# Kernel tuning notes

Measured on AMD Instinct MI355X. Metric: run time of the kernel, lower is better.

## Reference

```python
import jax, jax.numpy as jnp
import numpy as np

B, C, NS, NT = 8, 256, 16384, 2048
KQ = 64            # self-attention key/query dim
D = 64             # cond_conv_feat_dim
W0, W1, W2 = D * D, D * D, D * 1   # dynamic weight sizes (predict_mask=True)
B0, B1, B2 = D, D, 1
CTRL = W0 + W1 + W2 + B0 + B1 + B2  # 8385


def setup_inputs() -> dict:
    key = jax.random.key(0)
    ks = jax.random.split(key, 9)
    return {
        "scene_feat": jax.random.normal(ks[0], (B, C, NS), jnp.float32),
        "template_feat": jax.random.normal(ks[1], (B, C, NT), jnp.float32),
        # SelfAttention 1x1-conv (= linear over channels) weights
        "q_w": jax.random.normal(ks[2], (KQ, C), jnp.float32) * 0.02,
        "k_w": jax.random.normal(ks[3], (KQ, C), jnp.float32) * 0.02,
        "v_w": jax.random.normal(ks[4], (C, C), jnp.float32) * 0.02,
        # projection head of SimpleAggregator: Conv1d(3*C -> D, k=1) + ReLU
        "proj_w": jax.random.normal(ks[5], (D, 3 * C), jnp.float32) * 0.02,
        "proj_b": jnp.zeros((D,), jnp.float32),
        # controller head: Linear(C -> CTRL), init normal(std=0.01), bias 0
        "ctrl_w": jax.random.normal(ks[6], (CTRL, C), jnp.float32) * 0.01,
        "ctrl_b": jnp.zeros((CTRL,), jnp.float32),
    }


def _self_attention(x, q_w, k_w, v_w):
    # x: [B, C, N] -> [B, C_out, N]
    q = jnp.einsum("kc,bcn->bnk", q_w, x)          # [B, N, KQ]
    k = jnp.einsum("kc,bcn->bkn", k_w, x)          # [B, KQ, N]
    v = jnp.einsum("oc,bcn->bno", v_w, x)          # [B, N, C_out]
    attn = jax.nn.softmax(jnp.einsum("bnk,bkm->bnm", q / jnp.sqrt(jnp.float32(KQ)), k), axis=-1)
    y = jnp.einsum("bnm,bmo->bon", attn, v)        # [B, C_out, N]
    return y


def reference(scene_feat, template_feat, q_w, k_w, v_w, proj_w, proj_b, ctrl_w, ctrl_b):
    # ---- SimpleAggregator (self-attention on template inside) ----
    t_sa = _self_attention(template_feat, q_w, k_w, v_w)       # [B, C, NT]
    t_max = jnp.max(t_sa, axis=-1, keepdims=True)              # [B, C, 1]
    aggr = jnp.concatenate(
        [scene_feat - t_max, scene_feat * t_max, scene_feat], axis=1
    )                                                          # [B, 3C, NS]
    x = jax.nn.relu(jnp.einsum("oc,bcn->bon", proj_w, aggr) + proj_b[None, :, None])  # [B, D, NS]

    # ---- controller head on ORIGINAL template_feat max-pooled ----
    pooled = jnp.max(template_feat, axis=-1)                   # [B, C]
    params = pooled @ ctrl_w.T + ctrl_b                        # [B, CTRL]

    # parse_dynamic_params: splits = weights then biases
    o = 0
    w0 = params[:, o:o + W0].reshape(B, D, D); o += W0
    w1 = params[:, o:o + W1].reshape(B, D, D); o += W1
    w2 = params[:, o:o + W2].reshape(B, 1, D); o += W2
    b0 = params[:, o:o + B0]; o += B0
    b1 = params[:, o:o + B1]; o += B1
    b2 = params[:, o:o + B2]

    # per-sample dynamic 1x1 convs (groups=batch trick == batched GEMM)
    x = jax.nn.relu(jnp.einsum("boi,bin->bon", w0, x) + b0[:, :, None])
    x = jax.nn.relu(jnp.einsum("boi,bin->bon", w1, x) + b1[:, :, None])
    x = jnp.einsum("boi,bin->bon", w2, x) + b2[:, :, None]    # [B, 1, NS], no relu (mask layer)
    return x.reshape(B, NS)
```

## Files before the change

### kernel.cpp

```cpp
#include <hip/hip_runtime.h>
#include <hip/hip_fp8.h>


typedef __attribute__((ext_vector_type(8))) short short8;
typedef __attribute__((ext_vector_type(4))) short short4v;
typedef __attribute__((ext_vector_type(4))) float f32x4;
typedef __attribute__((ext_vector_type(8))) int int8v;

__device__ __forceinline__ unsigned short f2bf(float f){
  unsigned u = __float_as_uint(f);
  u += 0x7FFFu + ((u >> 16) & 1u);
  return (unsigned short)(u >> 16);
}
__device__ __forceinline__ unsigned char f2e4m3(float f){
  return __hip_fp8_e4m3(f).__x;
}
__device__ __forceinline__ unsigned fenc(float f){
  unsigned u = __float_as_uint(f);
  return (u & 0x80000000u) ? ~u : (u | 0x80000000u);
}
__device__ __forceinline__ float fdec(unsigned k){
  unsigned u = (k & 0x80000000u) ? (k & 0x7FFFFFFFu) : ~k;
  return __uint_as_float(u);
}

__global__ __launch_bounds__(256) void k0_tt(const float* __restrict__ T,
    unsigned short* __restrict__ Tt, unsigned* __restrict__ pooledEnc,
    const float* __restrict__ qw, const float* __restrict__ kw,
    const float* __restrict__ vw, unsigned short* __restrict__ Wbf){
  const int wg = blockIdx.x;
  const int tid = threadIdx.x;
  if (wg >= 1024){
    const int e = ((wg - 1024) * 256 + tid) * 4;
    const int row = e >> 8, c = e & 255;
    const float* src;
    float scl = 1.0f;
    if (row < 64){ src = qw + row * 256 + c; scl = 0.125f; }
    else if (row < 128){ src = kw + (row - 64) * 256 + c; }
    else { src = vw + (row - 128) * 256 + c; }
    float4 v = *(const float4*)src;
    short4v o;
    o[0] = (short)f2bf(v.x * scl); o[1] = (short)f2bf(v.y * scl);
    o[2] = (short)f2bf(v.z * scl); o[3] = (short)f2bf(v.w * scl);
    *(short4v*)(Wbf + e) = o;
    return;
  }
  const int b = wg & 7, nt = (wg >> 3) & 15, ct = wg >> 7;
  const int n0 = nt * 128, c0 = ct * 32;
  __shared__ float Ls[32][129];
  const int cr = tid >> 3, nq = tid & 7;
  const float* src = T + ((size_t)b * 256 + c0 + cr) * 2048 + n0 + nq * 16;
  float4 v0 = ((const float4*)src)[0];
  float4 v1 = ((const float4*)src)[1];
  float4 v2 = ((const float4*)src)[2];
  float4 v3 = ((const float4*)src)[3];
  float mx = fmaxf(fmaxf(fmaxf(v0.x, v0.y), fmaxf(v0.z, v0.w)),
                   fmaxf(fmaxf(v1.x, v1.y), fmaxf(v1.z, v1.w)));
  mx = fmaxf(mx, fmaxf(fmaxf(fmaxf(v2.x, v2.y), fmaxf(v2.z, v2.w)),
                       fmaxf(fmaxf(v3.x, v3.y), fmaxf(v3.z, v3.w))));
  mx = fmaxf(mx, __shfl_xor(mx, 1));
  mx = fmaxf(mx, __shfl_xor(mx, 2));
  mx = fmaxf(mx, __shfl_xor(mx, 4));
  if (nq == 0) atomicMax(&pooledEnc[b * 256 + c0 + cr], fenc(mx));
  float* lr = &Ls[cr][nq * 16];
  *(float4*)lr = v0; *(float4*)(lr + 4) = v1;
  *(float4*)(lr + 8) = v2; *(float4*)(lr + 12) = v3;
  __syncthreads();
  const int nr = tid >> 1, ch = tid & 1;
  unsigned short ob[16];
  #pragma unroll
  for (int j = 0; j < 16; j++) ob[j] = f2bf(Ls[ch * 16 + j][nr]);
  unsigned short* dst = Tt + ((size_t)b * 2048 + n0 + nr) * 256 + c0 + ch * 16;
  *(short8*)dst = *(short8*)&ob[0];
  *(short8*)(dst + 8) = *(short8*)&ob[8];
}

__global__ __launch_bounds__(256) void k23_qkv_params(
    const unsigned short* __restrict__ Wbf, const unsigned short* __restrict__ Tt,
    unsigned short* __restrict__ qo, unsigned short* __restrict__ ko,
    unsigned char* __restrict__ vt8,
    const unsigned* __restrict__ pooledEnc, const float* __restrict__ cw,
    const float* __restrict__ cb, float* __restrict__ params){
  const int wg = blockIdx.x;
  const int tid = threadIdx.x, lane = tid & 63, w = tid >> 6;
  if (wg >= 512){
    __shared__ float P[8 * 256];
    for (int i = tid; i < 2048; i += 256) P[i] = fdec(pooledEnc[i]);
    __syncthreads();
    const int r = (wg - 512) * 4 + w;
    if (r >= 8385) return;
    float4 c4 = ((const float4*)(cw + (size_t)r * 256))[lane];
    float bias = cb[r];
    #pragma unroll
    for (int b = 0; b < 8; b++){
      const float* pbp = P + b * 256 + lane * 4;
      float s = c4.x * pbp[0] + c4.y * pbp[1] + c4.z * pbp[2] + c4.w * pbp[3];
      #pragma unroll
      for (int d = 1; d < 64; d <<= 1) s += __shfl_xor(s, d);
      if (lane == 0) params[b * 8385 + r] = s + bias;
    }
    return;
  }
  const int b = wg & 7, nt = wg >> 3;
  const int n0 = nt * 32;
  const int l15 = lane & 15, g = lane >> 4;
  const unsigned short* Tb = Tt + (size_t)b * 2048 * 256;

  f32x4 aqk[2][2], av[4][2];
  #pragma unroll
  for (int i = 0; i < 2; i++)
    #pragma unroll
    for (int nf = 0; nf < 2; nf++) aqk[i][nf] = (f32x4){0.f,0.f,0.f,0.f};
  #pragma unroll
  for (int j = 0; j < 4; j++)
    #pragma unroll
    for (int nf = 0; nf < 2; nf++) av[j][nf] = (f32x4){0.f,0.f,0.f,0.f};

  #pragma unroll 2
  for (int kc = 0; kc < 8; kc++){
    short8 bfr[2];
    #pragma unroll
    for (int nf = 0; nf < 2; nf++)
      bfr[nf] = *(const short8*)(Tb + (size_t)(n0 + nf * 16 + l15) * 256 + kc * 32 + g * 8);
    short8 aq[2];
    #pragma unroll
    for (int i = 0; i < 2; i++)
      aq[i] = *(const short8*)(Wbf + (size_t)((2 * w + i) * 16 + l15) * 256 + kc * 32 + g * 8);
    short8 afv[4];
    #pragma unroll
    for (int j = 0; j < 4; j++)
      afv[j] = *(const short8*)(Wbf + (size_t)(128 + (4 * w + j) * 16 + l15) * 256 + kc * 32 + g * 8);
    #pragma unroll
    for (int i = 0; i < 2; i++)
      #pragma unroll
      for (int nf = 0; nf < 2; nf++)
        aqk[i][nf] = __builtin_amdgcn_mfma_f32_16x16x32_bf16(aq[i], bfr[nf], aqk[i][nf], 0, 0, 0);
    #pragma unroll
    for (int j = 0; j < 4; j++)
      #pragma unroll
      for (int nf = 0; nf < 2; nf++)
        av[j][nf] = __builtin_amdgcn_mfma_f32_16x16x32_bf16(bfr[nf], afv[j], av[j][nf], 0, 0, 0);
  }
  unsigned short* qk = (w < 2) ? qo : ko;
  #pragma unroll
  for (int i = 0; i < 2; i++)
    #pragma unroll
    for (int nf = 0; nf < 2; nf++){
      int n = n0 + nf * 16 + l15;
      int cbase = (w & 1) * 32 + i * 16 + g * 4;
      short4v pk;
      #pragma unroll
      for (int r = 0; r < 4; r++) pk[r] = (short)f2bf(aqk[i][nf][r]);
      *(short4v*)(qk + ((size_t)b * 2048 + n) * 64 + cbase) = pk;
    }
  #pragma unroll
  for (int j = 0; j < 4; j++)
    #pragma unroll
    for (int nf = 0; nf < 2; nf++){
      int o = (4 * w + j) * 16 + l15;
      int nb2 = n0 + nf * 16 + g * 4;
      unsigned pv8 = 0;
      #pragma unroll
      for (int r = 0; r < 4; r++)
        pv8 |= (unsigned)f2e4m3(av[j][nf][r]) << (8 * r);
      *(unsigned*)(vt8 + ((size_t)b * 256 + o) * 2048 + nb2) = pv8;
    }
}

__global__ __launch_bounds__(512, 4) void kA_scores(
    const unsigned short* __restrict__ Qg, const unsigned short* __restrict__ Kg,
    unsigned char* __restrict__ Pg, float* __restrict__ sbuf,
    int b0, int bshift){
  const int wg = blockIdx.x;
  const int bmask = (1 << bshift) - 1;
  const int b = b0 + (wg & bmask);
  const int q0 = (wg >> bshift) * 32;
  const int tid = threadIdx.x, lane = tid & 63, w = tid >> 6;
  const int l15 = lane & 15, g = lane >> 4;
  __shared__ float wsum[32][8];
  const unsigned short* Qb = Qg + (size_t)b * 2048 * 64;
  const unsigned short* Kb = Kg + (size_t)b * 2048 * 64;
  unsigned char* Pb = Pg + (size_t)(wg & bmask) * 2048 * 2048;

  short8 qf[2][2];
  #pragma unroll
  for (int qi = 0; qi < 2; qi++)
    #pragma unroll
    for (int kc = 0; kc < 2; kc++)
      qf[qi][kc] = *(const short8*)(Qb + (size_t)(q0 + qi * 16 + l15) * 64 + kc * 32 + g * 8);

  float ps[2] = {0.f, 0.f};

  const int wm0 = w * 256;
  #pragma unroll
  for (int mt = 0; mt < 4; ++mt){
    const int mb = wm0 + mt * 64;
    short8 kf[4][2];
    #pragma unroll
    for (int mi = 0; mi < 4; mi++)
      #pragma unroll
      for (int kc = 0; kc < 2; kc++)
        kf[mi][kc] = *(const short8*)(Kb + (size_t)(mb + mi * 16 + l15) * 64 + kc * 32 + g * 8);
    #pragma unroll
    for (int qi = 0; qi < 2; qi++){
      f32x4 sa[4];
      #pragma unroll
      for (int mi = 0; mi < 4; mi++) sa[mi] = (f32x4){0.f,0.f,0.f,0.f};
      #pragma unroll
      for (int mi = 0; mi < 4; mi++)
        #pragma unroll
        for (int kc = 0; kc < 2; kc++)
          sa[mi] = __builtin_amdgcn_mfma_f32_16x16x32_bf16(kf[mi][kc], qf[qi][kc], sa[mi], 0, 0, 0);
      #pragma unroll
      for (int mi = 0; mi < 4; mi++){
        unsigned pk8 = 0;
        #pragma unroll
        for (int r = 0; r < 4; r++){
          float p = __expf(sa[mi][r]);
          ps[qi] += p;
          pk8 |= (unsigned)f2e4m3(p) << (8 * r);
        }
        *(unsigned*)(Pb + (size_t)(q0 + qi * 16 + l15) * 2048 + mb + mi * 16 + g * 4) = pk8;
      }
    }
  }
  #pragma unroll
  for (int qi = 0; qi < 2; qi++){
    float t = ps[qi];
    t += __shfl_xor(t, 16);
    t += __shfl_xor(t, 32);
    if (lane < 16) wsum[qi * 16 + l15][w] = t;
  }
  __syncthreads();
  if (tid < 32){
    float t = 0.f;
    #pragma unroll
    for (int i = 0; i < 8; i++) t += wsum[tid][i];
    sbuf[(size_t)b * 2048 + q0 + tid] = t;
  }
}

__global__ __launch_bounds__(256, 3) void kB_pv(
    const unsigned char* __restrict__ Pg, const unsigned char* __restrict__ Vt,
    const float* __restrict__ sbuf, unsigned* __restrict__ tmaxe,
    int b0, int bshift){
  const int wg = blockIdx.x;
  const int bmask = (1 << bshift) - 1;
  const int b = b0 + (wg & bmask);
  const int rest = wg >> bshift;
  const int oh = rest & 1;
  const int n0 = (rest >> 1) * 64;
  const int tid = threadIdx.x, lane = tid & 63, w = tid >> 6;
  const int l15 = lane & 15, g = lane >> 4;
  __shared__ __align__(32) unsigned char smem[2][24576];

  const unsigned char* Pb = Pg + (size_t)(wg & bmask) * 2048 * 2048;
  const unsigned char* Vb = Vt + ((size_t)b * 256 + oh * 128) * 2048;

  f32x4 acc[4][2];
  #pragma unroll
  for (int ni = 0; ni < 4; ni++)
    #pragma unroll
    for (int oi = 0; oi < 2; oi++) acc[ni][oi] = (f32x4){0.f,0.f,0.f,0.f};

  const unsigned char* psrc[6];
  {
    #pragma unroll
    for (int k = 0; k < 6; k++){
      int d = k * 4096 + w * 1024 + lane * 16;
      if (k < 2){
        int row = d >> 7;
        int colB = (d & 127) ^ ((row & 3) << 5);
        psrc[k] = Pb + (size_t)(n0 + row) * 2048 + colB;
      } else {
        int dv = d - 8192;
        int row = dv >> 7;
        int colB = (dv & 127) ^ ((row & 3) << 5);
        psrc[k] = Vb + (size_t)row * 2048 + colB;
      }
    }
  }
  auto ISSUE = [&](int m0, int bufIdx){
    #pragma unroll
    for (int k = 0; k < 6; k++){
      unsigned char* dst = &smem[bufIdx][k * 4096 + w * 1024];
      __builtin_amdgcn_global_load_lds(
          (const __attribute__((address_space(1))) void*)(psrc[k] + m0),
          (__attribute__((address_space(3))) void*)dst, 16, 0, 0);
    }
  };

  ISSUE(0, 0);
  __syncthreads();

  const int SC = 0x7F7F7F7F;
  for (int t = 0; t < 16; ++t){
    unsigned char* cur = smem[t & 1];
    if (t < 15) ISSUE((t + 1) * 128, (t + 1) & 1);
    int8v af[4], bf[2];
    #pragma unroll
    for (int ni = 0; ni < 4; ni++){
      int row = ni * 16 + l15;
      af[ni] = *(const int8v*)(cur + row * 128 + ((g * 32) ^ ((row & 3) << 5)));
    }
    #pragma unroll
    for (int oi = 0; oi < 2; oi++){
      int row = w * 32 + oi * 16 + l15;
      bf[oi] = *(const int8v*)(cur + 8192 + row * 128 + ((g * 32) ^ ((row & 3) << 5)));
    }
    #pragma unroll
    for (int ni = 0; ni < 4; ni++)
      #pragma unroll
      for (int oi = 0; oi < 2; oi++)
        acc[ni][oi] = __builtin_amdgcn_mfma_scale_f32_16x16x128_f8f6f4(
            af[ni], bf[oi], acc[ni][oi], 0, 0, 0, SC, 0, SC);
    if (t < 15)
      __syncthreads();
  }
  float inv[4][4];
  #pragma unroll
  for (int ni = 0; ni < 4; ni++)
    #pragma unroll
    for (int r = 0; r < 4; r++)
      inv[ni][r] = 1.0f / sbuf[(size_t)b * 2048 + n0 + ni * 16 + g * 4 + r];
  #pragma unroll
  for (int oi = 0; oi < 2; oi++){
    float cm = -1e30f;
    #pragma unroll
    for (int ni = 0; ni < 4; ni++)
      #pragma unroll
      for (int r = 0; r < 4; r++)
        cm = fmaxf(cm, acc[ni][oi][r] * inv[ni][r]);
    cm = fmaxf(cm, __shfl_xor(cm, 16));
    cm = fmaxf(cm, __shfl_xor(cm, 32));
    if (lane < 16)
      atomicMax(&tmaxe[b * 256 + oh * 128 + w * 32 + oi * 16 + lane], fenc(cm));
  }
}

__global__ __launch_bounds__(256) void k5_weff(const float* __restrict__ proj_w,
    const float* __restrict__ proj_b, const unsigned* __restrict__ tmaxe,
    const float* __restrict__ params, unsigned short* __restrict__ weff,
    float* __restrict__ beff, unsigned short* __restrict__ w0b,
    unsigned short* __restrict__ w1b){
  const int b = blockIdx.y, o = blockIdx.x;
  const int c = threadIdx.x;
  float t = fdec(tmaxe[b * 256 + c]);
  float p0 = proj_w[o * 768 + c];
  float p1 = proj_w[o * 768 + 256 + c];
  float p2 = proj_w[o * 768 + 512 + c];
  weff[((size_t)b * 64 + o) * 256 + c] = f2bf(p0 + p1 * t + p2);
  float s = p0 * t;
  #pragma unroll
  for (int d = 1; d < 64; d <<= 1) s += __shfl_xor(s, d);
  __shared__ float sm[4];
  if ((c & 63) == 0) sm[c >> 6] = s;
  __syncthreads();
  if (c == 0) beff[b * 64 + o] = proj_b[o] - (sm[0] + sm[1] + sm[2] + sm[3]);
  if (c < 64)        w0b[((size_t)b * 64 + o) * 64 + c] = f2bf(params[b * 8385 + o * 64 + c]);
  else if (c < 128)  w1b[((size_t)b * 64 + o) * 64 + (c - 64)] = f2bf(params[b * 8385 + 4096 + o * 64 + (c - 64)]);
}

__global__ __launch_bounds__(512) void k6_main(const float* __restrict__ Sg,
    const unsigned short* __restrict__ weff, const float* __restrict__ beff,
    const unsigned short* __restrict__ w0b, const unsigned short* __restrict__ w1b,
    const float* __restrict__ params, float* __restrict__ out){
  const int b = blockIdx.y, nt = blockIdx.x;
  const int n0 = nt * 256;
  const int tid = threadIdx.x, lane = tid & 63, w = tid >> 6;
  const int l15 = lane & 15, g = lane >> 4;
  __shared__ __align__(16) unsigned char smem[65536];
  unsigned short* H0 = (unsigned short*)smem;
  unsigned char*  Ub = smem + 32768;
  unsigned short* H1 = (unsigned short*)Ub;

  const float* Sb = Sg + (size_t)b * 256 * 16384;
  const unsigned short* We = weff + (size_t)b * 64 * 256;
  f32x4 a0[4][2];
  #pragma unroll
  for (int mi = 0; mi < 4; mi++)
    #pragma unroll
    for (int ni = 0; ni < 2; ni++) a0[mi][ni] = (f32x4){0.f,0.f,0.f,0.f};

  const int scc = tid & 31;
  const int snb = (tid >> 5) * 16;
  const float* src0 = Sb + (size_t)scc * 16384 + n0 + snb;
  float4 v0 = ((const float4*)src0)[0];
  float4 v1 = ((const float4*)src0)[1];
  float4 v2 = ((const float4*)src0)[2];
  float4 v3 = ((const float4*)src0)[3];
  for (int k0 = 0; k0 < 256; k0 += 32){
    float vals[16] = {v0.x,v0.y,v0.z,v0.w, v1.x,v1.y,v1.z,v1.w,
                      v2.x,v2.y,v2.z,v2.w, v3.x,v3.y,v3.z,v3.w};
    #pragma unroll
    for (int j = 0; j < 16; j++){
      int n = snb + j;
      unsigned byteo = ((unsigned)(n * 64 + scc * 2)) ^ ((unsigned)((n >> 1) & 3) << 4);
      *(unsigned short*)(Ub + byteo) = f2bf(vals[j]);
    }
    if (k0 < 224){
      const float* nsrc = Sb + (size_t)(k0 + 32 + scc) * 16384 + n0 + snb;
      v0 = ((const float4*)nsrc)[0];
      v1 = ((const float4*)nsrc)[1];
      v2 = ((const float4*)nsrc)[2];
      v3 = ((const float4*)nsrc)[3];
    }
    __syncthreads();
    short8 bf0[2];
    #pragma unroll
    for (int ni = 0; ni < 2; ni++){
      int n = w * 32 + ni * 16 + l15;
      bf0[ni] = *(const short8*)(Ub + (((unsigned)(n * 64 + g * 16)) ^ ((unsigned)((n >> 1) & 3) << 4)));
    }
    #pragma unroll
    for (int mi = 0; mi < 4; mi++){
      short8 af = *(const short8*)(We + (mi * 16 + l15) * 256 + k0 + g * 8);
      #pragma unroll
      for (int ni = 0; ni < 2; ni++)
        a0[mi][ni] = __builtin_amdgcn_mfma_f32_16x16x32_bf16(af, bf0[ni], a0[mi][ni], 0, 0, 0);
    }
    __syncthreads();
  }
  const float* be = beff + b * 64;
  #pragma unroll
  for (int mi = 0; mi < 4; mi++)
    #pragma unroll
    for (int ni = 0; ni < 2; ni++){
      int n = w * 32 + ni * 16 + l15;
      unsigned base = ((unsigned)(n * 128 + mi * 32 + g * 8)) ^ ((unsigned)((n & 7) << 4));
      unsigned short hh[4];
      #pragma unroll
      for (int r = 0; r < 4; r++){
        int o = mi * 16 + g * 4 + r;
        hh[r] = f2bf(fmaxf(a0[mi][ni][r] + be[o], 0.f));
      }
      *(unsigned*)((unsigned char*)H0 + base)     = (unsigned)hh[0] | ((unsigned)hh[1] << 16);
      *(unsigned*)((unsigned char*)H0 + base + 4) = (unsigned)hh[2] | ((unsigned)hh[3] << 16);
    }
  __syncthreads();
  f32x4 a1[4][2];
  #pragma unroll
  for (int mi = 0; mi < 4; mi++)
    #pragma unroll
    for (int ni = 0; ni < 2; ni++) a1[mi][ni] = (f32x4){0.f,0.f,0.f,0.f};
  const unsigned short* W0 = w0b + (size_t)b * 4096;
  #pragma unroll
  for (int ks = 0; ks < 2; ks++){
    short8 bfh[2];
    #pragma unroll
    for (int ni = 0; ni < 2; ni++){
      int n = w * 32 + ni * 16 + l15;
      unsigned off = ((unsigned)(n * 128 + ks * 64 + g * 16)) ^ ((unsigned)((n & 7) << 4));
      bfh[ni] = *(const short8*)((unsigned char*)H0 + off);
    }
    #pragma unroll
    for (int mi = 0; mi < 4; mi++){
      short8 af = *(const short8*)(W0 + (mi * 16 + l15) * 64 + ks * 32 + g * 8);
      #pragma unroll
      for (int ni = 0; ni < 2; ni++)
        a1[mi][ni] = __builtin_amdgcn_mfma_f32_16x16x32_bf16(af, bfh[ni], a1[mi][ni], 0, 0, 0);
    }
  }
  const float* pp = params + (size_t)b * 8385;
  const float* b0p = pp + 8256;
  #pragma unroll
  for (int mi = 0; mi < 4; mi++)
    #pragma unroll
    for (int ni = 0; ni < 2; ni++){
      int n = w * 32 + ni * 16 + l15;
      unsigned base = ((unsigned)(n * 128 + mi * 32 + g * 8)) ^ ((unsigned)((n & 7) << 4));
      unsigned short hh[4];
      #pragma unroll
      for (int r = 0; r < 4; r++){
        int o = mi * 16 + g * 4 + r;
        hh[r] = f2bf(fmaxf(a1[mi][ni][r] + b0p[o], 0.f));
      }
      *(unsigned*)((unsigned char*)H1 + base)     = (unsigned)hh[0] | ((unsigned)hh[1] << 16);
      *(unsigned*)((unsigned char*)H1 + base + 4) = (unsigned)hh[2] | ((unsigned)hh[3] << 16);
    }
  __syncthreads();
  f32x4 a2[4][2];
  #pragma unroll
  for (int mi = 0; mi < 4; mi++)
    #pragma unroll
    for (int ni = 0; ni < 2; ni++) a2[mi][ni] = (f32x4){0.f,0.f,0.f,0.f};
  const unsigned short* W1 = w1b + (size_t)b * 4096;
  #pragma unroll
  for (int ks = 0; ks < 2; ks++){
    short8 bfh[2];
    #pragma unroll
    for (int ni = 0; ni < 2; ni++){
      int n = w * 32 + ni * 16 + l15;
      unsigned off = ((unsigned)(n * 128 + ks * 64 + g * 16)) ^ ((unsigned)((n & 7) << 4));
      bfh[ni] = *(const short8*)((unsigned char*)H1 + off);
    }
    #pragma unroll
    for (int mi = 0; mi < 4; mi++){
      short8 af = *(const short8*)(W1 + (mi * 16 + l15) * 64 + ks * 32 + g * 8);
      #pragma unroll
      for (int ni = 0; ni < 2; ni++)
        a2[mi][ni] = __builtin_amdgcn_mfma_f32_16x16x32_bf16(af, bfh[ni], a2[mi][ni], 0, 0, 0);
    }
  }
  const float* b1p = pp + 8320;
  const float* w2p = pp + 8192;
  float b2v = pp[8384];
  #pragma unroll
  for (int ni = 0; ni < 2; ni++){
    float t = 0.f;
    #pragma unroll
    for (int mi = 0; mi < 4; mi++)
      #pragma unroll
      for (int r = 0; r < 4; r++){
        int o = mi * 16 + g * 4 + r;
        t += w2p[o] * fmaxf(a2[mi][ni][r] + b1p[o], 0.f);
      }
    t += __shfl_xor(t, 16);
    t += __shfl_xor(t, 32);
    if (lane < 16)
      out[(size_t)b * 16384 + n0 + w * 32 + ni * 16 + l15] = t + b2v;
  }
}

extern "C" void kernel_launch(void* const* d_in, const int* in_sizes, int n_in,
                              void* d_out, int out_size, void* d_ws, size_t ws_size,
                              hipStream_t stream){
  const float* scene = (const float*)d_in[0];
  const float* tmpl  = (const float*)d_in[1];
  const float* qw    = (const float*)d_in[2];
  const float* kw    = (const float*)d_in[3];
  const float* vw    = (const float*)d_in[4];
  const float* pw    = (const float*)d_in[5];
  const float* pb    = (const float*)d_in[6];
  const float* cw    = (const float*)d_in[7];
  const float* cb    = (const float*)d_in[8];
  float* out = (float*)d_out;
  char* ws = (char*)d_ws;

  unsigned short* Q      = (unsigned short*)(ws + 0);
  unsigned short* K      = (unsigned short*)(ws + (2u << 20));
  unsigned char*  V8     = (unsigned char*)(ws + (4u << 20));
  unsigned*       pooledEnc = (unsigned*)(ws + (12u << 20));
  unsigned*       tmaxe  = (unsigned*)(ws + (12u << 20) + 8192);
  float*          params = (float*)(ws + (12u << 20) + 16384);
  unsigned short* w0b    = (unsigned short*)(ws + (13u << 20));
  unsigned short* w1b    = (unsigned short*)(ws + (13u << 20) + 65536);
  unsigned short* weff   = (unsigned short*)(ws + (13u << 20) + 131072);
  float*          beff   = (float*)(ws + (13u << 20) + 131072 + 262144);
  float*          sbuf   = (float*)(ws + (14u << 20));
  unsigned short* Wbf    = (unsigned short*)(ws + (14u << 20) + 131072);
  unsigned char*  P8buf  = (unsigned char*)(ws + (16u << 20));
  unsigned short* Tt     = (unsigned short*)P8buf;

  const size_t pPerBatch = (size_t)2048 * 2048;
  size_t avail = ws_size > (16u << 20) ? ws_size - (16u << 20) : 0;
  int nb = 8, bshift = 3;
  while (nb > 1 && (size_t)nb * pPerBatch > avail){ nb >>= 1; bshift--; }

  hipMemsetAsync(ws + (12u << 20), 0, 16384, stream);
  k0_tt<<<dim3(1120), dim3(256), 0, stream>>>(tmpl, Tt, pooledEnc, qw, kw, vw, Wbf);
  k23_qkv_params<<<dim3(512 + 2097), dim3(256), 0, stream>>>(Wbf, Tt, Q, K, V8,
                                                             pooledEnc, cw, cb, params);
  for (int b0 = 0; b0 < 8; b0 += nb){
    kA_scores<<<dim3(64 * nb), dim3(512), 0, stream>>>(Q, K, P8buf, sbuf, b0, bshift);
    kB_pv<<<dim3(64 * nb), dim3(256), 0, stream>>>(P8buf, V8, sbuf, tmaxe, b0, bshift);
  }
  k5_weff<<<dim3(64, 8), dim3(256), 0, stream>>>(pw, pb, tmaxe, params, weff, beff, w0b, w1b);
  k6_main<<<dim3(64, 8), dim3(512), 0, stream>>>(scene, weff, beff, w0b, w1b, params, out);
}
```

Before: 130.7 us.

## Pre-transpose scene to bf16 channel-last and simplify main kernel staging

```diff
diff --git a/kernel.cpp b/kernel.cpp
--- a/kernel.cpp
+++ b/kernel.cpp
@@ -75,6 +75,32 @@
   *(short8*)(dst + 8) = *(short8*)&ob[8];
 }
 
+__global__ __launch_bounds__(256) void kT_scene(const float* __restrict__ S,
+    unsigned short* __restrict__ St){
+  const int wg = blockIdx.x;
+  const int b = wg & 7, nt = (wg >> 3) & 127, ct = wg >> 10;
+  const int n0 = nt * 128, c0 = ct * 32;
+  const int tid = threadIdx.x;
+  __shared__ float Ls[32][129];
+  const int cr = tid >> 3, nq = tid & 7;
+  const float* src = S + ((size_t)b * 256 + c0 + cr) * 16384 + n0 + nq * 16;
+  float4 v0 = ((const float4*)src)[0];
+  float4 v1 = ((const float4*)src)[1];
+  float4 v2 = ((const float4*)src)[2];
+  float4 v3 = ((const float4*)src)[3];
+  float* lr = &Ls[cr][nq * 16];
+  *(float4*)lr = v0; *(float4*)(lr + 4) = v1;
+  *(float4*)(lr + 8) = v2; *(float4*)(lr + 12) = v3;
+  __syncthreads();
+  const int nr = tid >> 1, ch = tid & 1;
+  unsigned short ob[16];
+  #pragma unroll
+  for (int j = 0; j < 16; j++) ob[j] = f2bf(Ls[ch * 16 + j][nr]);
+  unsigned short* dst = St + ((size_t)b * 16384 + n0 + nr) * 256 + c0 + ch * 16;
+  *(short8*)dst = *(short8*)&ob[0];
+  *(short8*)(dst + 8) = *(short8*)&ob[8];
+}
+
 __global__ __launch_bounds__(256) void k23_qkv_params(
     const unsigned short* __restrict__ Wbf, const unsigned short* __restrict__ Tt,
     unsigned short* __restrict__ qo, unsigned short* __restrict__ ko,
@@ -340,9 +366,7 @@
 
 __global__ __launch_bounds__(256) void k5_weff(const float* __restrict__ proj_w,
     const float* __restrict__ proj_b, const unsigned* __restrict__ tmaxe,
-    const float* __restrict__ params, unsigned short* __restrict__ weff,
-    float* __restrict__ beff, unsigned short* __restrict__ w0b,
-    unsigned short* __restrict__ w1b){
+    unsigned short* __restrict__ weff, float* __restrict__ beff){
   const int b = blockIdx.y, o = blockIdx.x;
   const int c = threadIdx.x;
   float t = fdec(tmaxe[b * 256 + c]);
@@ -357,24 +381,21 @@
   if ((c & 63) == 0) sm[c >> 6] = s;
   __syncthreads();
   if (c == 0) beff[b * 64 + o] = proj_b[o] - (sm[0] + sm[1] + sm[2] + sm[3]);
-  if (c < 64)        w0b[((size_t)b * 64 + o) * 64 + c] = f2bf(params[b * 8385 + o * 64 + c]);
-  else if (c < 128)  w1b[((size_t)b * 64 + o) * 64 + (c - 64)] = f2bf(params[b * 8385 + 4096 + o * 64 + (c - 64)]);
-}
-
-__global__ __launch_bounds__(512) void k6_main(const float* __restrict__ Sg,
+}
+
+__global__ __launch_bounds__(256) void k6_main(const unsigned short* __restrict__ St,
     const unsigned short* __restrict__ weff, const float* __restrict__ beff,
-    const unsigned short* __restrict__ w0b, const unsigned short* __restrict__ w1b,
     const float* __restrict__ params, float* __restrict__ out){
-  const int b = blockIdx.y, nt = blockIdx.x;
-  const int n0 = nt * 256;
+  const int wg = blockIdx.x;
+  const int b = wg & 7, nt = wg >> 3;
+  const int n0 = nt * 128;
   const int tid = threadIdx.x, lane = tid & 63, w = tid >> 6;
   const int l15 = lane & 15, g = lane >> 4;
-  __shared__ __align__(16) unsigned char smem[65536];
+  __shared__ __align__(16) unsigned char smem[32768];
   unsigned short* H0 = (unsigned short*)smem;
-  unsigned char*  Ub = smem + 32768;
-  unsigned short* H1 = (unsigned short*)Ub;
-
-  const float* Sb = Sg + (size_t)b * 256 * 16384;
+  unsigned short* H1 = (unsigned short*)(smem + 16384);
+
+  const unsigned short* Stb = St + ((size_t)b * 16384 + n0) * 256;
   const unsigned short* We = weff + (size_t)b * 64 * 256;
   f32x4 a0[4][2];
   #pragma unroll
@@ -382,44 +403,21 @@
     #pragma unroll
     for (int ni = 0; ni < 2; ni++) a0[mi][ni] = (f32x4){0.f,0.f,0.f,0.f};
 
-  const int scc = tid & 31;
-  const int snb = (tid >> 5) * 16;
-  const float* src0 = Sb + (size_t)scc * 16384 + n0 + snb;
-  float4 v0 = ((const float4*)src0)[0];
-  float4 v1 = ((const float4*)src0)[1];
-  float4 v2 = ((const float4*)src0)[2];
-  float4 v3 = ((const float4*)src0)[3];
-  for (int k0 = 0; k0 < 256; k0 += 32){
-    float vals[16] = {v0.x,v0.y,v0.z,v0.w, v1.x,v1.y,v1.z,v1.w,
-                      v2.x,v2.y,v2.z,v2.w, v3.x,v3.y,v3.z,v3.w};
-    #pragma unroll
-    for (int j = 0; j < 16; j++){
-      int n = snb + j;
-      unsigned byteo = ((unsigned)(n * 64 + scc * 2)) ^ ((unsigned)((n >> 1) & 3) << 4);
-      *(unsigned short*)(Ub + byteo) = f2bf(vals[j]);
-    }
-    if (k0 < 224){
-      const float* nsrc = Sb + (size_t)(k0 + 32 + scc) * 16384 + n0 + snb;
-      v0 = ((const float4*)nsrc)[0];
-      v1 = ((const float4*)nsrc)[1];
-      v2 = ((const float4*)nsrc)[2];
-      v3 = ((const float4*)nsrc)[3];
-    }
-    __syncthreads();
+  #pragma unroll
+  for (int kc = 0; kc < 8; kc++){
     short8 bf0[2];
     #pragma unroll
     for (int ni = 0; ni < 2; ni++){
       int n = w * 32 + ni * 16 + l15;
-      bf0[ni] = *(const short8*)(Ub + (((unsigned)(n * 64 + g * 16)) ^ ((unsigned)((n >> 1) & 3) << 4)));
+      bf0[ni] = *(const short8*)(Stb + (size_t)n * 256 + kc * 32 + g * 8);
     }
     #pragma unroll
     for (int mi = 0; mi < 4; mi++){
-      short8 af = *(const short8*)(We + (mi * 16 + l15) * 256 + k0 + g * 8);
+      short8 af = *(const short8*)(We + (size_t)(mi * 16 + l15) * 256 + kc * 32 + g * 8);
       #pragma unroll
       for (int ni = 0; ni < 2; ni++)
         a0[mi][ni] = __builtin_amdgcn_mfma_f32_16x16x32_bf16(af, bf0[ni], a0[mi][ni], 0, 0, 0);
     }
-    __syncthreads();
   }
   const float* be = beff + b * 64;
   #pragma unroll
@@ -438,12 +436,12 @@
       *(unsigned*)((unsigned char*)H0 + base + 4) = (unsigned)hh[2] | ((unsigned)hh[3] << 16);
     }
   __syncthreads();
+  const float* pp = params + (size_t)b * 8385;
   f32x4 a1[4][2];
   #pragma unroll
   for (int mi = 0; mi < 4; mi++)
     #pragma unroll
     for (int ni = 0; ni < 2; ni++) a1[mi][ni] = (f32x4){0.f,0.f,0.f,0.f};
-  const unsigned short* W0 = w0b + (size_t)b * 4096;
   #pragma unroll
   for (int ks = 0; ks < 2; ks++){
     short8 bfh[2];
@@ -455,13 +453,19 @@
     }
     #pragma unroll
     for (int mi = 0; mi < 4; mi++){
-      short8 af = *(const short8*)(W0 + (mi * 16 + l15) * 64 + ks * 32 + g * 8);
+      const float* wsrc = pp + (mi * 16 + l15) * 64 + ks * 32 + g * 8;
+      float4 x0 = *(const float4*)wsrc;
+      float4 x1 = *(const float4*)(wsrc + 4);
+      short8 af;
+      af[0] = (short)f2bf(x0.x); af[1] = (short)f2bf(x0.y);
+      af[2] = (short)f2bf(x0.z); af[3] = (short)f2bf(x0.w);
+      af[4] = (short)f2bf(x1.x); af[5] = (short)f2bf(x1.y);
+      af[6] = (short)f2bf(x1.z); af[7] = (short)f2bf(x1.w);
       #pragma unroll
       for (int ni = 0; ni < 2; ni++)
         a1[mi][ni] = __builtin_amdgcn_mfma_f32_16x16x32_bf16(af, bfh[ni], a1[mi][ni], 0, 0, 0);
     }
   }
-  const float* pp = params + (size_t)b * 8385;
   const float* b0p = pp + 8256;
   #pragma unroll
   for (int mi = 0; mi < 4; mi++)
@@ -484,7 +488,6 @@
   for (int mi = 0; mi < 4; mi++)
     #pragma unroll
     for (int ni = 0; ni < 2; ni++) a2[mi][ni] = (f32x4){0.f,0.f,0.f,0.f};
-  const unsigned short* W1 = w1b + (size_t)b * 4096;
   #pragma unroll
   for (int ks = 0; ks < 2; ks++){
     short8 bfh[2];
@@ -496,7 +499,14 @@
     }
     #pragma unroll
     for (int mi = 0; mi < 4; mi++){
-      short8 af = *(const short8*)(W1 + (mi * 16 + l15) * 64 + ks * 32 + g * 8);
+      const float* wsrc = pp + 4096 + (mi * 16 + l15) * 64 + ks * 32 + g * 8;
+      float4 x0 = *(const float4*)wsrc;
+      float4 x1 = *(const float4*)(wsrc + 4);
+      short8 af;
+      af[0] = (short)f2bf(x0.x); af[1] = (short)f2bf(x0.y);
+      af[2] = (short)f2bf(x0.z); af[3] = (short)f2bf(x0.w);
+      af[4] = (short)f2bf(x1.x); af[5] = (short)f2bf(x1.y);
+      af[6] = (short)f2bf(x1.z); af[7] = (short)f2bf(x1.w);
       #pragma unroll
       for (int ni = 0; ni < 2; ni++)
         a2[mi][ni] = __builtin_amdgcn_mfma_f32_16x16x32_bf16(af, bfh[ni], a2[mi][ni], 0, 0, 0);
@@ -543,14 +553,13 @@
   unsigned*       pooledEnc = (unsigned*)(ws + (12u << 20));
   unsigned*       tmaxe  = (unsigned*)(ws + (12u << 20) + 8192);
   float*          params = (float*)(ws + (12u << 20) + 16384);
-  unsigned short* w0b    = (unsigned short*)(ws + (13u << 20));
-  unsigned short* w1b    = (unsigned short*)(ws + (13u << 20) + 65536);
-  unsigned short* weff   = (unsigned short*)(ws + (13u << 20) + 131072);
-  float*          beff   = (float*)(ws + (13u << 20) + 131072 + 262144);
+  unsigned short* weff   = (unsigned short*)(ws + (13u << 20));
+  float*          beff   = (float*)(ws + (13u << 20) + 262144);
   float*          sbuf   = (float*)(ws + (14u << 20));
   unsigned short* Wbf    = (unsigned short*)(ws + (14u << 20) + 131072);
   unsigned char*  P8buf  = (unsigned char*)(ws + (16u << 20));
   unsigned short* Tt     = (unsigned short*)P8buf;
+  unsigned short* St     = (unsigned short*)P8buf;
 
   const size_t pPerBatch = (size_t)2048 * 2048;
   size_t avail = ws_size > (16u << 20) ? ws_size - (16u << 20) : 0;
@@ -565,6 +574,7 @@
     kA_scores<<<dim3(64 * nb), dim3(512), 0, stream>>>(Q, K, P8buf, sbuf, b0, bshift);
     kB_pv<<<dim3(64 * nb), dim3(256), 0, stream>>>(P8buf, V8, sbuf, tmaxe, b0, bshift);
   }
-  k5_weff<<<dim3(64, 8), dim3(256), 0, stream>>>(pw, pb, tmaxe, params, weff, beff, w0b, w1b);
-  k6_main<<<dim3(64, 8), dim3(512), 0, stream>>>(scene, weff, beff, w0b, w1b, params, out);
-}
+  kT_scene<<<dim3(8192), dim3(256), 0, stream>>>(scene, St);
+  k5_weff<<<dim3(64, 8), dim3(256), 0, stream>>>(pw, pb, tmaxe, weff, beff);
+  k6_main<<<dim3(1024), dim3(256), 0, stream>>>(St, weff, beff, params, out);
+}
```

Measured after the change: 167.6 us. 28.2% more time.
